# Kernel optimization log

Hardware: AMD Instinct MI355X
Metric: run time of the kernel (lower is better)

Reference implementation:

```python
import jax, jax.numpy as jnp
import numpy as np

B, C, H, W = 16, 256, 96, 96   # img_feat dims; C == image_feat_channel
FG, TFC = 64, 128              # feature_groups, text_feat_channel
EPS = 1e-5                     # BatchNorm eps (torch default)


def setup_inputs() -> dict:
    key = jax.random.key(0)
    ks = jax.random.split(key, 4)
    return {
        "img_feat": jax.random.normal(ks[0], (B, C, H, W), jnp.float32),
        "text_feat": jax.random.normal(ks[1], (B, TFC), jnp.float32),
        # ConvTranspose2d weights use torch layout (in, out, kh, kw)
        "w1": jax.random.normal(ks[2], (TFC, FG, 4, 4), jnp.float32) * 0.05,
        "b1": jnp.zeros((FG,), jnp.float32),
        "gamma1": jnp.ones((FG,), jnp.float32),
        "beta1": jnp.zeros((FG,), jnp.float32),
        "w2": jax.random.normal(ks[3], (FG, FG, 4, 4), jnp.float32) * 0.05,
        "b2": jnp.zeros((FG,), jnp.float32),
        "gamma2": jnp.ones((FG,), jnp.float32),
        "beta2": jnp.zeros((FG,), jnp.float32),
    }


def _bn(x, gamma, beta):
    # BatchNorm2d in training mode: batch statistics over (N, H, W)
    m = x.mean(axis=(0, 2, 3), keepdims=True)
    v = x.var(axis=(0, 2, 3), keepdims=True)
    return (x - m) * jax.lax.rsqrt(v + EPS) * gamma[None, :, None, None] + beta[None, :, None, None]


def reference(img_feat, text_feat, w1, b1, gamma1, beta1, w2, b2, gamma2, beta2):
    b, c, h, w = img_feat.shape
    # UnFlatten(1): [b,TFC] -> [b,TFC,1,1]; ConvTranspose2d(TFC,FG,4,1,0) on a
    # 1x1 input is just an outer product with the 4x4 kernel -> [b,FG,4,4]
    t = jnp.einsum('bc,coij->boij', text_feat, w1) + b1[None, :, None, None]
    t = jax.nn.relu(_bn(t, gamma1, beta1))
    # ConvTranspose2d(FG,FG,4,stride=2,pad=1): 4x4 -> 8x8.
    # Equivalent dilated conv: flip kernel spatially, swap in/out -> OIHW,
    # lhs_dilation=2, pad = k-1-p = 2 per side.
    w2f = jnp.flip(w2, (-2, -1)).swapaxes(0, 1)  # (out, in, 4, 4)
    t = jax.lax.conv_general_dilated(
        t, w2f, window_strides=(1, 1), padding=((2, 2), (2, 2)),
        lhs_dilation=(2, 2), dimension_numbers=('NCHW', 'OIHW', 'NCHW'))
    t = t + b2[None, :, None, None]
    t = jax.nn.relu(_bn(t, gamma2, beta2))  # [b, FG, 8, 8]
    # repeat each template c//FG times across channels -> per-channel kernels
    rep = c // FG
    kern = jnp.broadcast_to(t[:, :, None], (b, FG, rep, 8, 8)).reshape(b * c, 1, 8, 8)
    # per-sample per-channel depthwise cross-correlation, stride 4
    y = jax.lax.conv_general_dilated(
        img_feat.reshape(1, b * c, h, w), kern, window_strides=(4, 4),
        padding='VALID', feature_group_count=b * c,
        dimension_numbers=('NCHW', 'OIHW', 'NCHW'))  # [1, b*c, oh, ow]
    # adaptive_max_pool2d(..., 1) == global spatial max
    out = jnp.max(y.reshape(b, c, -1), axis=-1)
    return jax.nn.relu(out) / 64.0
```

## Files before the change

kernel.cpp:

```cpp
#include <hip/hip_runtime.h>
#include <hip/hip_bf16.h>


#define EPSF 1e-5f

typedef unsigned short u16;
typedef unsigned int u32;

static __device__ __forceinline__ float blo(u32 u) { return __uint_as_float(u << 16); }
static __device__ __forceinline__ float bhi(u32 u) { return __uint_as_float(u & 0xffff0000u); }
static __device__ __forceinline__ int wild16(u32 u) {
    u32 e = (u >> 7) & 0xffu;
    return (e >= 134u) || (e >= 1u && e <= 90u);
}
static __device__ __forceinline__ int detect_fp32(const u32* p, size_t base,
                                                  int t, float* red4) {
    u32 u = p[base + t];
    float cnt = (float)(wild16(u & 0xffffu) + wild16(u >> 16));
    #pragma unroll
    for (int m = 1; m < 64; m <<= 1) cnt += __shfl_xor(cnt, m, 64);
    if ((t & 63) == 0) red4[t >> 6] = cnt;
    __syncthreads();
    float tot = red4[0] + red4[1] + red4[2] + red4[3];
    __syncthreads();
    return tot > 64.f;
}

#define OFF_TEXT  0
#define OFF_W1    2048
#define OFF_W2    133120
#define OFF_G1    198656
#define OFF_BE1   198720
#define OFF_G2    198784
#define OFF_BE2   198848
#define OFF_T1    198912
#define OFF_T2    215296
#define CVT_N     198912

__global__ __launch_bounds__(256) void k_cvt(const void* __restrict__ text,
                                             const void* __restrict__ w1,
                                             const void* __restrict__ w2,
                                             const void* __restrict__ g1,
                                             const void* __restrict__ be1,
                                             const void* __restrict__ g2,
                                             const void* __restrict__ be2,
                                             float* __restrict__ ws) {
    __shared__ float red4[4];
    int t = threadIdx.x;
    int isf32 = detect_fp32((const u32*)text, 0, t, red4);

    int eidx = (blockIdx.x * 256 + t) * 4;
    if (eidx >= CVT_N) return;
    const void* src; int soff;
    if (eidx < 2048)        { src = text; soff = eidx; }
    else if (eidx < 133120) { src = w1;   soff = eidx - 2048; }
    else if (eidx < 198656) { src = w2;   soff = eidx - 133120; }
    else {
        int k = eidx - 198656;
        int which = k >> 6;
        soff = k & 63;
        src = (which == 0) ? g1 : (which == 1) ? be1 : (which == 2) ? g2 : be2;
    }
    float4 v;
    if (isf32) {
        v = ((const float4*)src)[soff >> 2];
    } else {
        uint2 q = *(const uint2*)((const u16*)src + soff);
        v.x = blo(q.x); v.y = bhi(q.x); v.z = blo(q.y); v.w = bhi(q.y);
    }
    *(float4*)(ws + eidx) = v;
}

__global__ __launch_bounds__(256) void k_t1(const float* __restrict__ ws,
                                            float* __restrict__ tmpl1) {
    __shared__ float r1[4], r2[4];
    const float* textf = ws + OFF_TEXT;
    const float* w1f   = ws + OFF_W1;
    int o = blockIdx.x, t = threadIdx.x;
    int b = t >> 4, s = t & 15;
    const float* tr = textf + b * 128;
    const float* wr = w1f + o * 16 + s;
    float acc = 0.f;
    #pragma unroll 4
    for (int c = 0; c < 128; ++c)
        acc += tr[c] * wr[c * 1024];

    float s1 = acc, s2 = acc * acc;
    #pragma unroll
    for (int m = 1; m < 64; m <<= 1) {
        s1 += __shfl_xor(s1, m, 64);
        s2 += __shfl_xor(s2, m, 64);
    }
    if ((t & 63) == 0) { r1[t >> 6] = s1; r2[t >> 6] = s2; }
    __syncthreads();
    s1 = r1[0] + r1[1] + r1[2] + r1[3];
    s2 = r2[0] + r2[1] + r2[2] + r2[3];
    float mean = s1 * (1.f / 256.f);
    float var  = s2 * (1.f / 256.f) - mean * mean;
    float scale = ws[OFF_G1 + o] * rsqrtf(var + EPSF);
    float shift = ws[OFF_BE1 + o] - mean * scale;
    tmpl1[b * 1024 + s * 64 + o] = fmaxf(acc * scale + shift, 0.f);
}

__global__ __launch_bounds__(64) void k_ct(const float* __restrict__ ws,
                                           float* __restrict__ t2) {
    __shared__ float st1[1024];
    __shared__ float sw2[17 * 64];
    const float* tmpl1 = ws + OFF_T1;
    const float* w2f   = ws + OFF_W2;
    int bx = blockIdx.x;
    int b = bx >> 6, o = bx & 63;
    int t = threadIdx.x;

    {
        const float4* src = (const float4*)(tmpl1 + b * 1024);
        float4* dst = (float4*)st1;
        #pragma unroll
        for (int j = 0; j < 4; ++j) dst[t + j * 64] = src[t + j * 64];
    }
    {
        const float4* wp = (const float4*)(w2f + (t * 64 + o) * 16);
        #pragma unroll
        for (int q = 0; q < 4; ++q) {
            float4 w4 = wp[q];
            sw2[(4 * q + 0) * 64 + t] = w4.x;
            sw2[(4 * q + 1) * 64 + t] = w4.y;
            sw2[(4 * q + 2) * 64 + t] = w4.z;
            sw2[(4 * q + 3) * 64 + t] = w4.w;
        }
        sw2[16 * 64 + t] = 0.f;
    }
    __syncthreads();

    int y = t >> 3, x = t & 7;
    int iy0 = (y - 1) >> 1; if (iy0 < 0) iy0 = 0;
    int ix0 = (x - 1) >> 1; if (ix0 < 0) ix0 = 0;
    float acc = 0.f;
    #pragma unroll
    for (int u = 0; u < 2; ++u) {
        int iy = iy0 + u, ky = y + 1 - 2 * iy;
        bool vy = (ky >= 0) && (iy <= 3);
        int iyc = iy > 3 ? 3 : iy;
        #pragma unroll
        for (int v = 0; v < 2; ++v) {
            int ix = ix0 + v, kx = x + 1 - 2 * ix;
            bool vx = (kx >= 0) && (ix <= 3);
            int ixc = ix > 3 ? 3 : ix;
            int arow = iyc * 4 + ixc;
            int krow = (vy && vx) ? (ky * 4 + kx) : 16;
            const float4* a4 = (const float4*)(st1 + arow * 64);
            const float4* w4 = (const float4*)(sw2 + krow * 64);
            #pragma unroll
            for (int i = 0; i < 16; ++i) {
                float4 av = a4[i], wv = w4[i];
                acc += av.x * wv.x + av.y * wv.y + av.z * wv.z + av.w * wv.w;
            }
        }
    }
    t2[o * 1024 + b * 64 + t] = acc;
}

__global__ __launch_bounds__(256) void k_bn2(float* __restrict__ t2,
                                             const float* __restrict__ ws) {
    __shared__ float r1[4], r2[4];
    int o = blockIdx.x, t = threadIdx.x;
    float4* p = (float4*)(t2 + o * 1024);
    float4 v = p[t];
    float s1 = v.x + v.y + v.z + v.w;
    float s2 = v.x * v.x + v.y * v.y + v.z * v.z + v.w * v.w;
    #pragma unroll
    for (int m = 1; m < 64; m <<= 1) {
        s1 += __shfl_xor(s1, m, 64);
        s2 += __shfl_xor(s2, m, 64);
    }
    if ((t & 63) == 0) { r1[t >> 6] = s1; r2[t >> 6] = s2; }
    __syncthreads();
    s1 = r1[0] + r1[1] + r1[2] + r1[3];
    s2 = r2[0] + r2[1] + r2[2] + r2[3];
    float mean = s1 * (1.f / 1024.f);
    float var  = s2 * (1.f / 1024.f) - mean * mean;
    float scale = ws[OFF_G2 + o] * rsqrtf(var + EPSF);
    float shift = ws[OFF_BE2 + o] - mean * scale;
    v.x = fmaxf(v.x * scale + shift, 0.f);
    v.y = fmaxf(v.y * scale + shift, 0.f);
    v.z = fmaxf(v.z * scale + shift, 0.f);
    v.w = fmaxf(v.w * scale + shift, 0.f);
    p[t] = v;
}

__global__ __launch_bounds__(256) void k_corr(const void* __restrict__ img,
                                              const float* __restrict__ t2,
                                              float* __restrict__ out) {
    __shared__ float sf[96 * 100];
    __shared__ float sk[64];
    __shared__ float red4[4];
    int bc = blockIdx.x;
    int b = bc >> 8, c = bc & 255, o = c >> 2;
    int t = threadIdx.x;

    int isf32 = detect_fp32((const u32*)img, (size_t)bc * 4608, t, red4);

    if (t < 64) sk[t] = t2[(o * 16 + b) * 64 + t];

    if (isf32) {
        const uint4* src = (const uint4*)((const float*)img + (size_t)bc * 9216);
        #pragma unroll
        for (int j = 0; j < 9; ++j) {
            int i = t + j * 256;
            uint4 q = src[i];
            int g = i * 4;
            int r = g / 96, cc = g - r * 96;
            float4* d = (float4*)(sf + r * 100 + cc);
            d[0] = make_float4(__uint_as_float(q.x), __uint_as_float(q.y),
                               __uint_as_float(q.z), __uint_as_float(q.w));
        }
    } else {
        const uint4* src = (const uint4*)((const u16*)img + (size_t)bc * 9216);
        #pragma unroll
        for (int j = 0; j < 5; ++j) {
            int i = t + j * 256;
            if (i < 1152) {
                uint4 q = src[i];
                int g = i * 8;
                int r = g / 96, cc = g - r * 96;
                float4* d = (float4*)(sf + r * 100 + cc);
                d[0] = make_float4(blo(q.x), bhi(q.x), blo(q.y), bhi(q.y));
                d[1] = make_float4(blo(q.z), bhi(q.z), blo(q.w), bhi(q.w));
            }
        }
    }
    __syncthreads();

    float vmax = 0.f;
    for (int p = t; p < 529; p += 256) {
        int oy = p / 23;
        int ox = p - oy * 23;
        const float* base = sf + oy * 400 + ox * 4;
        float acc = 0.f;
        #pragma unroll
        for (int dy = 0; dy < 8; ++dy) {
            const float* r = base + dy * 100;
            float4 a0 = *(const float4*)r;
            float4 a1 = *(const float4*)(r + 4);
            const float* kr = sk + dy * 8;
            acc += a0.x * kr[0] + a0.y * kr[1] + a0.z * kr[2] + a0.w * kr[3];
            acc += a1.x * kr[4] + a1.y * kr[5] + a1.z * kr[6] + a1.w * kr[7];
        }
        vmax = fmaxf(vmax, acc);
    }
    #pragma unroll
    for (int m = 1; m < 64; m <<= 1) vmax = fmaxf(vmax, __shfl_xor(vmax, m, 64));
    __syncthreads();
    if ((t & 63) == 0) red4[t >> 6] = vmax;
    __syncthreads();
    if (t == 0) {
        float r = fmaxf(fmaxf(red4[0], red4[1]), fmaxf(red4[2], red4[3]));
        out[bc] = fmaxf(r, 0.f) * (1.f / 64.f);
    }
}

extern "C" void kernel_launch(void* const* d_in, const int* in_sizes, int n_in,
                              void* d_out, int out_size, void* d_ws, size_t ws_size,
                              hipStream_t stream) {
    const void* img = nullptr; const void* text = nullptr;
    const void* w1 = nullptr;  const void* w2 = nullptr;
    const void* v64[6] = {nullptr, nullptr, nullptr, nullptr, nullptr, nullptr};
    int nv = 0;
    for (int i = 0; i < n_in; ++i) {
        int s = in_sizes[i];
        if      (s == 37748736) img  = d_in[i];
        else if (s == 2048)     text = d_in[i];
        else if (s == 131072)   w1   = d_in[i];
        else if (s == 65536)    w2   = d_in[i];
        else if (s == 64 && nv < 6) v64[nv++] = d_in[i];
    }
    const void* g1  = v64[1]; const void* be1 = v64[2];
    const void* g2  = v64[4]; const void* be2 = v64[5];

    float* ws = (float*)d_ws;
    float* tmpl1 = ws + OFF_T1;
    float* t2    = ws + OFF_T2;
    float* out = (float*)d_out;

    k_cvt <<<195,  256, 0, stream>>>(text, w1, w2, g1, be1, g2, be2, ws);
    k_t1  <<<64,   256, 0, stream>>>(ws, tmpl1);
    k_ct  <<<1024, 64,  0, stream>>>(ws, t2);
    k_bn2 <<<64,   256, 0, stream>>>(t2, ws);
    k_corr<<<4096, 256, 0, stream>>>(img, t2, out);
}
```

Baseline: 250.7 us.

## Drop dtype detection and conversion kernel, fuse transposed conv with BN2

Removes the runtime bf16/fp32 detection and the separate conversion kernel, so inputs are read directly as fp32. The transposed conv is fused with the second BatchNorm into one kernel per output channel, with the template and weights staged in shared memory. The correlation kernel moves to 512 threads per block and the text GEMV stages its operands in LDS. This cuts two launches and the detection passes, but assumes fp32 inputs and lowers the block count in the conv stage.

```diff
diff --git a/kernel.cpp b/kernel.cpp
--- a/kernel.cpp
+++ b/kernel.cpp
@@ -1,89 +1,44 @@
 #include <hip/hip_runtime.h>
-#include <hip/hip_bf16.h>
 
 
 #define EPSF 1e-5f
 
-typedef unsigned short u16;
-typedef unsigned int u32;
-
-static __device__ __forceinline__ float blo(u32 u) { return __uint_as_float(u << 16); }
-static __device__ __forceinline__ float bhi(u32 u) { return __uint_as_float(u & 0xffff0000u); }
-static __device__ __forceinline__ int wild16(u32 u) {
-    u32 e = (u >> 7) & 0xffu;
-    return (e >= 134u) || (e >= 1u && e <= 90u);
-}
-static __device__ __forceinline__ int detect_fp32(const u32* p, size_t base,
-                                                  int t, float* red4) {
-    u32 u = p[base + t];
-    float cnt = (float)(wild16(u & 0xffffu) + wild16(u >> 16));
-    #pragma unroll
-    for (int m = 1; m < 64; m <<= 1) cnt += __shfl_xor(cnt, m, 64);
-    if ((t & 63) == 0) red4[t >> 6] = cnt;
-    __syncthreads();
-    float tot = red4[0] + red4[1] + red4[2] + red4[3];
-    __syncthreads();
-    return tot > 64.f;
-}
-
-#define OFF_TEXT  0
-#define OFF_W1    2048
-#define OFF_W2    133120
-#define OFF_G1    198656
-#define OFF_BE1   198720
-#define OFF_G2    198784
-#define OFF_BE2   198848
-#define OFF_T1    198912
-#define OFF_T2    215296
-#define CVT_N     198912
-
-__global__ __launch_bounds__(256) void k_cvt(const void* __restrict__ text,
-                                             const void* __restrict__ w1,
-                                             const void* __restrict__ w2,
-                                             const void* __restrict__ g1,
-                                             const void* __restrict__ be1,
-                                             const void* __restrict__ g2,
-                                             const void* __restrict__ be2,
-                                             float* __restrict__ ws) {
-    __shared__ float red4[4];
-    int t = threadIdx.x;
-    int isf32 = detect_fp32((const u32*)text, 0, t, red4);
-
-    int eidx = (blockIdx.x * 256 + t) * 4;
-    if (eidx >= CVT_N) return;
-    const void* src; int soff;
-    if (eidx < 2048)        { src = text; soff = eidx; }
-    else if (eidx < 133120) { src = w1;   soff = eidx - 2048; }
-    else if (eidx < 198656) { src = w2;   soff = eidx - 133120; }
-    else {
-        int k = eidx - 198656;
-        int which = k >> 6;
-        soff = k & 63;
-        src = (which == 0) ? g1 : (which == 1) ? be1 : (which == 2) ? g2 : be2;
-    }
-    float4 v;
-    if (isf32) {
-        v = ((const float4*)src)[soff >> 2];
-    } else {
-        uint2 q = *(const uint2*)((const u16*)src + soff);
-        v.x = blo(q.x); v.y = bhi(q.x); v.z = blo(q.y); v.w = bhi(q.y);
-    }
-    *(float4*)(ws + eidx) = v;
-}
-
-__global__ __launch_bounds__(256) void k_t1(const float* __restrict__ ws,
+__global__ __launch_bounds__(256) void k_t1(const float* __restrict__ textf,
+                                            const float* __restrict__ w1f,
+                                            const float* __restrict__ g1,
+                                            const float* __restrict__ be1,
                                             float* __restrict__ tmpl1) {
+    __shared__ float stext[128 * 17];
+    __shared__ float sw1[128 * 17];
     __shared__ float r1[4], r2[4];
-    const float* textf = ws + OFF_TEXT;
-    const float* w1f   = ws + OFF_W1;
     int o = blockIdx.x, t = threadIdx.x;
+
+    #pragma unroll
+    for (int j = 0; j < 2; ++j) {
+        int i4 = t + 256 * j;
+        float4 v = ((const float4*)textf)[i4];
+        int e = i4 * 4, b = e >> 7, c = e & 127;
+        stext[(c + 0) * 17 + b] = v.x;
+        stext[(c + 1) * 17 + b] = v.y;
+        stext[(c + 2) * 17 + b] = v.z;
+        stext[(c + 3) * 17 + b] = v.w;
+    }
+    #pragma unroll
+    for (int j = 0; j < 2; ++j) {
+        int c = (t >> 2) + 64 * j, q = t & 3;
+        float4 v = *(const float4*)(w1f + c * 1024 + o * 16 + q * 4);
+        sw1[c * 17 + q * 4 + 0] = v.x;
+        sw1[c * 17 + q * 4 + 1] = v.y;
+        sw1[c * 17 + q * 4 + 2] = v.z;
+        sw1[c * 17 + q * 4 + 3] = v.w;
+    }
+    __syncthreads();
+
     int b = t >> 4, s = t & 15;
-    const float* tr = textf + b * 128;
-    const float* wr = w1f + o * 16 + s;
     float acc = 0.f;
-    #pragma unroll 4
+    #pragma unroll 8
     for (int c = 0; c < 128; ++c)
-        acc += tr[c] * wr[c * 1024];
+        acc += stext[c * 17 + b] * sw1[c * 17 + s];
 
     float s1 = acc, s2 = acc * acc;
     #pragma unroll
@@ -97,45 +52,45 @@
     s2 = r2[0] + r2[1] + r2[2] + r2[3];
     float mean = s1 * (1.f / 256.f);
     float var  = s2 * (1.f / 256.f) - mean * mean;
-    float scale = ws[OFF_G1 + o] * rsqrtf(var + EPSF);
-    float shift = ws[OFF_BE1 + o] - mean * scale;
+    float scale = g1[o] * rsqrtf(var + EPSF);
+    float shift = be1[o] - mean * scale;
     tmpl1[b * 1024 + s * 64 + o] = fmaxf(acc * scale + shift, 0.f);
 }
 
-__global__ __launch_bounds__(64) void k_ct(const float* __restrict__ ws,
-                                           float* __restrict__ t2) {
-    __shared__ float st1[1024];
-    __shared__ float sw2[17 * 64];
-    const float* tmpl1 = ws + OFF_T1;
-    const float* w2f   = ws + OFF_W2;
-    int bx = blockIdx.x;
-    int b = bx >> 6, o = bx & 63;
-    int t = threadIdx.x;
-
-    {
-        const float4* src = (const float4*)(tmpl1 + b * 1024);
-        float4* dst = (float4*)st1;
-        #pragma unroll
-        for (int j = 0; j < 4; ++j) dst[t + j * 64] = src[t + j * 64];
-    }
-    {
-        const float4* wp = (const float4*)(w2f + (t * 64 + o) * 16);
-        #pragma unroll
-        for (int q = 0; q < 4; ++q) {
-            float4 w4 = wp[q];
-            sw2[(4 * q + 0) * 64 + t] = w4.x;
-            sw2[(4 * q + 1) * 64 + t] = w4.y;
-            sw2[(4 * q + 2) * 64 + t] = w4.z;
-            sw2[(4 * q + 3) * 64 + t] = w4.w;
-        }
-        sw2[16 * 64 + t] = 0.f;
-    }
-    __syncthreads();
-
-    int y = t >> 3, x = t & 7;
+__global__ __launch_bounds__(512) void k_ctbn(const float* __restrict__ tmpl1,
+                                              const float* __restrict__ w2f,
+                                              const float* __restrict__ g2,
+                                              const float* __restrict__ be2,
+                                              float* __restrict__ t2) {
+    __shared__ float st1[256 * 68];
+    __shared__ float sw2[17 * 68];
+    __shared__ float r1[8], r2[8];
+    int o = blockIdx.x, t = threadIdx.x;
+
+    #pragma unroll
+    for (int j = 0; j < 8; ++j) {
+        int i4 = t + 512 * j;
+        float4 v = ((const float4*)tmpl1)[i4];
+        int e = i4 * 4;
+        int row = e >> 6, col = e & 63;
+        *(float4*)(st1 + row * 68 + col) = v;
+    }
+    if (t < 256) {
+        int i = t >> 2, q = t & 3;
+        float4 v = *(const float4*)(w2f + (i * 64 + o) * 16 + q * 4);
+        sw2[(q * 4 + 0) * 68 + i] = v.x;
+        sw2[(q * 4 + 1) * 68 + i] = v.y;
+        sw2[(q * 4 + 2) * 68 + i] = v.z;
+        sw2[(q * 4 + 3) * 68 + i] = v.w;
+    }
+    if (t < 68) sw2[16 * 68 + t] = 0.f;
+    __syncthreads();
+
+    int yx = t & 63, bq = t >> 6;
+    int y = yx >> 3, x = yx & 7;
     int iy0 = (y - 1) >> 1; if (iy0 < 0) iy0 = 0;
     int ix0 = (x - 1) >> 1; if (ix0 < 0) ix0 = 0;
-    float acc = 0.f;
+    float acc0 = 0.f, acc1 = 0.f;
     #pragma unroll
     for (int u = 0; u < 2; ++u) {
         int iy = iy0 + u, ky = y + 1 - 2 * iy;
@@ -148,26 +103,21 @@
             int ixc = ix > 3 ? 3 : ix;
             int arow = iyc * 4 + ixc;
             int krow = (vy && vx) ? (ky * 4 + kx) : 16;
-            const float4* a4 = (const float4*)(st1 + arow * 64);
-            const float4* w4 = (const float4*)(sw2 + krow * 64);
+            const float* a0 = st1 + ((bq * 2 + 0) * 16 + arow) * 68;
+            const float* a1 = st1 + ((bq * 2 + 1) * 16 + arow) * 68;
+            const float* w  = sw2 + krow * 68;
             #pragma unroll
             for (int i = 0; i < 16; ++i) {
-                float4 av = a4[i], wv = w4[i];
-                acc += av.x * wv.x + av.y * wv.y + av.z * wv.z + av.w * wv.w;
+                float4 wv  = *(const float4*)(w  + i * 4);
+                float4 av0 = *(const float4*)(a0 + i * 4);
+                float4 av1 = *(const float4*)(a1 + i * 4);
+                acc0 += av0.x * wv.x + av0.y * wv.y + av0.z * wv.z + av0.w * wv.w;
+                acc1 += av1.x * wv.x + av1.y * wv.y + av1.z * wv.z + av1.w * wv.w;
             }
         }
     }
-    t2[o * 1024 + b * 64 + t] = acc;
-}
-
-__global__ __launch_bounds__(256) void k_bn2(float* __restrict__ t2,
-                                             const float* __restrict__ ws) {
-    __shared__ float r1[4], r2[4];
-    int o = blockIdx.x, t = threadIdx.x;
-    float4* p = (float4*)(t2 + o * 1024);
-    float4 v = p[t];
-    float s1 = v.x + v.y + v.z + v.w;
-    float s2 = v.x * v.x + v.y * v.y + v.z * v.z + v.w * v.w;
+
+    float s1 = acc0 + acc1, s2 = acc0 * acc0 + acc1 * acc1;
     #pragma unroll
     for (int m = 1; m < 64; m <<= 1) {
         s1 += __shfl_xor(s1, m, 64);
@@ -175,64 +125,44 @@
     }
     if ((t & 63) == 0) { r1[t >> 6] = s1; r2[t >> 6] = s2; }
     __syncthreads();
-    s1 = r1[0] + r1[1] + r1[2] + r1[3];
-    s2 = r2[0] + r2[1] + r2[2] + r2[3];
+    s1 = 0.f; s2 = 0.f;
+    #pragma unroll
+    for (int k = 0; k < 8; ++k) { s1 += r1[k]; s2 += r2[k]; }
     float mean = s1 * (1.f / 1024.f);
     float var  = s2 * (1.f / 1024.f) - mean * mean;
-    float scale = ws[OFF_G2 + o] * rsqrtf(var + EPSF);
-    float shift = ws[OFF_BE2 + o] - mean * scale;
-    v.x = fmaxf(v.x * scale + shift, 0.f);
-    v.y = fmaxf(v.y * scale + shift, 0.f);
-    v.z = fmaxf(v.z * scale + shift, 0.f);
-    v.w = fmaxf(v.w * scale + shift, 0.f);
-    p[t] = v;
-}
-
-__global__ __launch_bounds__(256) void k_corr(const void* __restrict__ img,
+    float scale = g2[o] * rsqrtf(var + EPSF);
+    float shift = be2[o] - mean * scale;
+    t2[o * 1024 + (bq * 2 + 0) * 64 + yx] = fmaxf(acc0 * scale + shift, 0.f);
+    t2[o * 1024 + (bq * 2 + 1) * 64 + yx] = fmaxf(acc1 * scale + shift, 0.f);
+}
+
+__global__ __launch_bounds__(512) void k_corr(const float* __restrict__ img,
                                               const float* __restrict__ t2,
                                               float* __restrict__ out) {
     __shared__ float sf[96 * 100];
     __shared__ float sk[64];
-    __shared__ float red4[4];
+    __shared__ float red[8];
     int bc = blockIdx.x;
-    int b = bc >> 8, c = bc & 255, o = c >> 2;
+    int b = bc >> 8, o = (bc & 255) >> 2;
     int t = threadIdx.x;
 
-    int isf32 = detect_fp32((const u32*)img, (size_t)bc * 4608, t, red4);
-
     if (t < 64) sk[t] = t2[(o * 16 + b) * 64 + t];
 
-    if (isf32) {
-        const uint4* src = (const uint4*)((const float*)img + (size_t)bc * 9216);
-        #pragma unroll
-        for (int j = 0; j < 9; ++j) {
-            int i = t + j * 256;
-            uint4 q = src[i];
+    const float4* src = (const float4*)(img + (size_t)bc * 9216);
+    #pragma unroll
+    for (int j = 0; j < 5; ++j) {
+        int i = t + j * 512;
+        if (i < 2304) {
+            float4 v = src[i];
             int g = i * 4;
             int r = g / 96, cc = g - r * 96;
-            float4* d = (float4*)(sf + r * 100 + cc);
-            d[0] = make_float4(__uint_as_float(q.x), __uint_as_float(q.y),
-                               __uint_as_float(q.z), __uint_as_float(q.w));
+            *(float4*)(sf + r * 100 + cc) = v;
         }
-    } else {
-        const uint4* src = (const uint4*)((const u16*)img + (size_t)bc * 9216);
-        #pragma unroll
-        for (int j = 0; j < 5; ++j) {
-            int i = t + j * 256;
-            if (i < 1152) {
-                uint4 q = src[i];
-                int g = i * 8;
-                int r = g / 96, cc = g - r * 96;
-                float4* d = (float4*)(sf + r * 100 + cc);
-                d[0] = make_float4(blo(q.x), bhi(q.x), blo(q.y), bhi(q.y));
-                d[1] = make_float4(blo(q.z), bhi(q.z), blo(q.w), bhi(q.w));
-            }
-        }
     }
     __syncthreads();
 
     float vmax = 0.f;
-    for (int p = t; p < 529; p += 256) {
+    for (int p = t; p < 529; p += 512) {
         int oy = p / 23;
         int ox = p - oy * 23;
         const float* base = sf + oy * 400 + ox * 4;
@@ -250,11 +180,12 @@
     }
     #pragma unroll
     for (int m = 1; m < 64; m <<= 1) vmax = fmaxf(vmax, __shfl_xor(vmax, m, 64));
-    __syncthreads();
-    if ((t & 63) == 0) red4[t >> 6] = vmax;
+    if ((t & 63) == 0) red[t >> 6] = vmax;
     __syncthreads();
     if (t == 0) {
-        float r = fmaxf(fmaxf(red4[0], red4[1]), fmaxf(red4[2], red4[3]));
+        float r = red[0];
+        #pragma unroll
+        for (int k = 1; k < 8; ++k) r = fmaxf(r, red[k]);
         out[bc] = fmaxf(r, 0.f) * (1.f / 64.f);
     }
 }
@@ -262,29 +193,27 @@
 extern "C" void kernel_launch(void* const* d_in, const int* in_sizes, int n_in,
                               void* d_out, int out_size, void* d_ws, size_t ws_size,
                               hipStream_t stream) {
-    const void* img = nullptr; const void* text = nullptr;
-    const void* w1 = nullptr;  const void* w2 = nullptr;
-    const void* v64[6] = {nullptr, nullptr, nullptr, nullptr, nullptr, nullptr};
+    const float* img = nullptr; const float* text = nullptr;
+    const float* w1 = nullptr;  const float* w2 = nullptr;
+    const float* v64[6] = {nullptr, nullptr, nullptr, nullptr, nullptr, nullptr};
     int nv = 0;
     for (int i = 0; i < n_in; ++i) {
         int s = in_sizes[i];
-        if      (s == 37748736) img  = d_in[i];
-        else if (s == 2048)     text = d_in[i];
-        else if (s == 131072)   w1   = d_in[i];
-        else if (s == 65536)    w2   = d_in[i];
-        else if (s == 64 && nv < 6) v64[nv++] = d_in[i];
-    }
-    const void* g1  = v64[1]; const void* be1 = v64[2];
-    const void* g2  = v64[4]; const void* be2 = v64[5];
+        if      (s == 37748736) img  = (const float*)d_in[i];
+        else if (s == 2048)     text = (const float*)d_in[i];
+        else if (s == 131072)   w1   = (const float*)d_in[i];
+        else if (s == 65536)    w2   = (const float*)d_in[i];
+        else if (s == 64 && nv < 6) v64[nv++] = (const float*)d_in[i];
+    }
+    const float* g1  = v64[1]; const float* be1 = v64[2];
+    const float* g2  = v64[4]; const float* be2 = v64[5];
 
     float* ws = (float*)d_ws;
-    float* tmpl1 = ws + OFF_T1;
-    float* t2    = ws + OFF_T2;
+    float* tmpl1 = ws;
+    float* t2    = ws + 16384;
     float* out = (float*)d_out;
 
-    k_cvt <<<195,  256, 0, stream>>>(text, w1, w2, g1, be1, g2, be2, ws);
-    k_t1  <<<64,   256, 0, stream>>>(ws, tmpl1);
-    k_ct  <<<1024, 64,  0, stream>>>(ws, t2);
-    k_bn2 <<<64,   256, 0, stream>>>(t2, ws);
-    k_corr<<<4096, 256, 0, stream>>>(img, t2, out);
-}
+    k_t1  <<<64,   256, 0, stream>>>(text, w1, g1, be1, tmpl1);
+    k_ctbn<<<64,   512, 0, stream>>>(tmpl1, w2, g2, be2, t2);
+    k_corr<<<4096, 512, 0, stream>>>(img, t2, out);
+}
```

New measurement: 237.3 us. 1.06x faster.
